# Optimization experiments

Hardware: AMD Instinct MI355X
Metric: run time of the kernel (lower is better)

## Reference

```python
import jax, jax.numpy as jnp
import numpy as np

N = 100000   # nodes
E = 1600000  # edges (avg degree 16)
IN, HID, OUT, HEADS = 8, 32, 16, 4


def setup_inputs() -> dict:
    key = jax.random.key(0)
    ks = jax.random.split(key, 12)
    def g(k, shape, fan):
        return (jax.random.normal(k, shape, jnp.float32) / np.float32(np.sqrt(fan)))
    x = jax.random.normal(ks[0], (N, IN), jnp.float32)
    edge_index = jax.random.randint(ks[1], (2, E), 0, N, dtype=jnp.int64)
    return {
        "x": x,
        "edge_index": edge_index,
        "W1": g(ks[2], (IN, HEADS * HID), IN),
        "att_src1": g(ks[3], (HEADS, HID), HID),
        "att_dst1": g(ks[4], (HEADS, HID), HID),
        "b1": jnp.zeros((HEADS * HID,), jnp.float32),
        "W2": g(ks[5], (HEADS * HID, OUT), HEADS * HID),
        "att_src2": g(ks[6], (1, OUT), OUT),
        "att_dst2": g(ks[7], (1, OUT), OUT),
        "b2": jnp.zeros((OUT,), jnp.float32),
        "Wc1": g(ks[8], (OUT, 8), OUT),
        "bc1": jnp.zeros((8,), jnp.float32),
        "Wc2": g(ks[9], (8, 1), 8),
        "bc2": jnp.zeros((1,), jnp.float32),
    }


def _gat_layer(x, W, att_src, att_dst, bias, src, dst, n, concat):
    """PyG GATConv (eval mode): gather -> per-edge attention -> segment softmax -> scatter."""
    H, D = att_src.shape
    h = (x @ W).reshape(n, H, D)                       # [N,H,D]
    a_s = jnp.einsum("nhd,hd->nh", h, att_src)          # [N,H]
    a_d = jnp.einsum("nhd,hd->nh", h, att_dst)          # [N,H]
    e = jax.nn.leaky_relu(a_s[src] + a_d[dst], 0.2)     # [Etot,H]
    m = jax.ops.segment_max(e, dst, num_segments=n)     # per-dst max for stable softmax
    m = jnp.where(jnp.isfinite(m), m, 0.0)
    e = jnp.exp(e - m[dst])
    denom = jax.ops.segment_sum(e, dst, num_segments=n)
    alpha = e / (denom[dst] + 1e-16)                    # [Etot,H]
    out = jax.ops.segment_sum(h[src] * alpha[:, :, None], dst, num_segments=n)  # [N,H,D]
    out = out.reshape(n, H * D) if concat else out.mean(axis=1)
    return out + bias


def reference(x, edge_index, W1, att_src1, att_dst1, b1, W2, att_src2, att_dst2, b2, Wc1, bc1, Wc2, bc2):
    n = x.shape[0]
    loops = jnp.arange(n, dtype=edge_index.dtype)       # add_self_loops=True (PyG default)
    src = jnp.concatenate([edge_index[0], loops])
    dst = jnp.concatenate([edge_index[1], loops])
    h = jax.nn.elu(_gat_layer(x, W1, att_src1, att_dst1, b1, src, dst, n, concat=True))
    emb = jax.nn.elu(_gat_layer(h, W2, att_src2, att_dst2, b2, src, dst, n, concat=False))
    risk = jax.nn.sigmoid(jax.nn.relu(emb @ Wc1 + bc1) @ Wc2 + bc2)
    return emb, risk
```

## Files before the change

### kernel.cpp

```cpp
#include <hip/hip_runtime.h>
#include <hip/hip_fp16.h>
#include <math.h>

#define N_NODES 100000
#define N_EDGES 1600000
#define F_IN 8
#define HID 32
#define HEADS 4
#define F1 128
#define F2 16
#define NB 391
#define NBLK_BIN 782
#define EDGES_PER_BIN 2048
#define NBLK_A 391
#define BCAP 4864

__device__ __forceinline__ float leaky(float x){ return x > 0.f ? x : 0.2f * x; }
__device__ __forceinline__ float elu1(float x){ return x > 0.f ? x : __expf(x) - 1.f; }

__global__ __launch_bounds__(256) void k_bin_attn(
    const int* __restrict__ src, const int* __restrict__ dst,
    int* __restrict__ bucketCnt, unsigned int* __restrict__ ebuf,
    const float* __restrict__ x, const float* __restrict__ W1,
    const float* __restrict__ as1w, const float* __restrict__ ad1w,
    float* __restrict__ xa){
    __shared__ float smem[1344];
    int t = threadIdx.x;
    if (blockIdx.x < NBLK_BIN){
        int* hist    = (int*)smem;
        int* basePos = hist + NB;
        int* cur     = basePos + NB;
        for (int j = t; j < NB; j += 256) hist[j] = 0;
        __syncthreads();
        int base = blockIdx.x * EDGES_PER_BIN;
        int dv[8];
        #pragma unroll
        for (int j = 0; j < 8; j++){
            int e = base + j * 256 + t;
            dv[j] = (e < N_EDGES) ? dst[e] : -1;
            if (dv[j] >= 0) atomicAdd(&hist[dv[j] >> 8], 1);
        }
        __syncthreads();
        for (int j = t; j < NB; j += 256){
            int h = hist[j];
            if (h) basePos[j] = atomicAdd(&bucketCnt[j], h);
            cur[j] = 0;
        }
        __syncthreads();
        #pragma unroll
        for (int j = 0; j < 8; j++){
            if (dv[j] >= 0){
                int e = base + j * 256 + t;
                int d = dv[j];
                int b = d >> 8;
                int off = atomicAdd(&cur[b], 1);
                ebuf[b * BCAP + basePos[b] + off] = ((unsigned)(d & 255) << 17) | (unsigned)src[e];
            }
        }
    } else {
        float* W1s  = smem;
        float* atts = smem + 1024;
        float* attd = smem + 1152;
        float* cs   = smem + 1280;
        float* cd   = smem + 1312;
        ((float4*)W1s)[t] = ((const float4*)W1)[t];
        if (t < 128){ atts[t] = as1w[t]; attd[t] = ad1w[t]; }
        __syncthreads();
        if (t < 64){
            int m = t & 7, h = (t >> 3) & 3;
            bool sel = t >= 32;
            const float* wrow = W1s + m * F1 + h * 32;
            const float* av   = (sel ? attd : atts) + h * 32;
            float s = 0.f;
            #pragma unroll
            for (int d = 0; d < 32; d++) s += wrow[d] * av[d];
            (sel ? cd : cs)[h * 8 + m] = s;
        }
        __syncthreads();
        int n = (blockIdx.x - NBLK_BIN) * 256 + t;
        if (n < N_NODES){
            float4 x0 = ((const float4*)x)[n * 2];
            float4 x1 = ((const float4*)x)[n * 2 + 1];
            float4 osv, odv;
            float* po = (float*)&osv;
            float* pd = (float*)&odv;
            #pragma unroll
            for (int h = 0; h < 4; h++){
                const float* c0 = cs + h * 8;
                const float* c1 = cd + h * 8;
                po[h] = x0.x*c0[0] + x0.y*c0[1] + x0.z*c0[2] + x0.w*c0[3]
                      + x1.x*c0[4] + x1.y*c0[5] + x1.z*c0[6] + x1.w*c0[7];
                pd[h] = x0.x*c1[0] + x0.y*c1[1] + x0.z*c1[2] + x0.w*c1[3]
                      + x1.x*c1[4] + x1.y*c1[5] + x1.z*c1[6] + x1.w*c1[7];
            }
            float* px = xa + (size_t)n * 16;
            *(float4*)(px)      = x0;
            *(float4*)(px + 4)  = x1;
            *(float4*)(px + 8)  = osv;
            *(float4*)(px + 12) = odv;
        }
    }
}

__global__ __launch_bounds__(512) void k_local_csr(
    const int* __restrict__ bucketCnt, const unsigned int* __restrict__ ebuf,
    int* __restrict__ row_ptr, int* __restrict__ esrc){
    __shared__ int deg[256];
    __shared__ int scn[512];
    __shared__ int cntAll[NB];
    __shared__ unsigned int segs[BCAP];
    int b = blockIdx.x, t = threadIdx.x;
    if (t < 256) deg[t] = 0;
    for (int j = t; j < NB; j += 512) cntAll[j] = bucketCnt[j];
    __syncthreads();
    int partial = 0;
    for (int j = t; j < b; j += 512) partial += cntAll[j];
    scn[t] = partial;
    __syncthreads();
    for (int off = 256; off > 0; off >>= 1){
        if (t < off) scn[t] += scn[t + off];
        __syncthreads();
    }
    int sbase = scn[0];
    int cnt = cntAll[b];
    __syncthreads();
    const unsigned int* seg = ebuf + b * BCAP;
    for (int i = t; i < cnt; i += 512){
        unsigned int e = seg[i];
        segs[i] = e;
        atomicAdd(&deg[e >> 17], 1);
    }
    __syncthreads();
    int v = (t < 256) ? deg[t] : 0;
    if (t < 256) scn[t] = v;
    __syncthreads();
    for (int off = 1; off < 256; off <<= 1){
        int xx = (t < 256 && t >= off) ? scn[t - off] : 0;
        __syncthreads();
        if (t < 256) scn[t] += xx;
        __syncthreads();
    }
    if (t < 256){
        int excl = scn[t] - v;
        int start = sbase + excl;
        int n = b * 256 + t;
        if (n < N_NODES) row_ptr[n] = start;
        deg[t] = start;
    }
    if (b == NB - 1 && t == 0) row_ptr[N_NODES] = sbase + cnt;
    __syncthreads();
    for (int i = t; i < cnt; i += 512){
        unsigned int e = segs[i];
        int pos = atomicAdd(&deg[e >> 17], 1);
        esrc[pos] = (int)(e & 0x1FFFFu);
    }
}

__global__ __launch_bounds__(256) void k_agg1(
    const float* __restrict__ xa, const int* __restrict__ row_ptr, const int* __restrict__ esrc,
    float* __restrict__ xagg, float* __restrict__ dden){
    int t = threadIdx.x;
    int wv = t >> 6, lane = t & 63;
    int n = blockIdx.x * 4 + wv;
    int g = lane >> 4;
    int l = lane & 15;
    int hd = l >> 2;
    int c2 = (l & 3) * 2;

    float vn = xa[(size_t)n * 16 + l];
    float adh = __shfl(vn, 12 + hd, 16);

    float den = 0.f, ac0 = 0.f, ac1 = 0.f;
    if (g == 0){
        float w = __expf(leaky(__shfl(vn, 8 + hd, 16) + adh));
        den = w;
        ac0 = w * __shfl(vn, c2, 16);
        ac1 = w * __shfl(vn, c2 + 1, 16);
    }
    int start = row_ptr[n], end = row_ptr[n + 1];
    int len = end - start;
    int chunk = (len + 3) >> 2;
    int i = start + g * chunk;
    int e = i + chunk; if (e > end) e = end;
    for (int base = i; base < e; base += 4){
        bool b1v = base + 1 < e, b2v = base + 2 < e, b3v = base + 3 < e;
        int s0 = esrc[base];
        int s1 = b1v ? esrc[base + 1] : s0;
        int s2 = b2v ? esrc[base + 2] : s0;
        int s3 = b3v ? esrc[base + 3] : s0;
        float v0 = xa[(size_t)s0 * 16 + l];
        float v1 = xa[(size_t)s1 * 16 + l];
        float v2 = xa[(size_t)s2 * 16 + l];
        float v3 = xa[(size_t)s3 * 16 + l];
        float w0 = __expf(leaky(__shfl(v0, 8 + hd, 16) + adh));
        float w1 = b1v ? __expf(leaky(__shfl(v1, 8 + hd, 16) + adh)) : 0.f;
        float w2 = b2v ? __expf(leaky(__shfl(v2, 8 + hd, 16) + adh)) : 0.f;
        float w3 = b3v ? __expf(leaky(__shfl(v3, 8 + hd, 16) + adh)) : 0.f;
        den += (w0 + w1) + (w2 + w3);
        ac0 = fmaf(w0, __shfl(v0, c2, 16), ac0); ac1 = fmaf(w0, __shfl(v0, c2 + 1, 16), ac1);
        ac0 = fmaf(w1, __shfl(v1, c2, 16), ac0); ac1 = fmaf(w1, __shfl(v1, c2 + 1, 16), ac1);
        ac0 = fmaf(w2, __shfl(v2, c2, 16), ac0); ac1 = fmaf(w2, __shfl(v2, c2 + 1, 16), ac1);
        ac0 = fmaf(w3, __shfl(v3, c2, 16), ac0); ac1 = fmaf(w3, __shfl(v3, c2 + 1, 16), ac1);
    }
    den += __shfl_xor(den, 16); den += __shfl_xor(den, 32);
    ac0 += __shfl_xor(ac0, 16); ac0 += __shfl_xor(ac0, 32);
    ac1 += __shfl_xor(ac1, 16); ac1 += __shfl_xor(ac1, 32);

    if (lane < 16){
        float2 o; o.x = ac0; o.y = ac1;
        *(float2*)(xagg + (size_t)n * 32 + 2 * l) = o;
        if ((l & 3) == 0) dden[(size_t)n * 4 + hd] = den;
    }
}

__global__ __launch_bounds__(256) void k_epi(
    const float* __restrict__ xagg, const float* __restrict__ dden,
    const float* __restrict__ W1, const float* __restrict__ W2,
    const float* __restrict__ b1, const float* __restrict__ as2w, const float* __restrict__ ad2w,
    __half* __restrict__ h2h, float* __restrict__ a_s2, float* __restrict__ a_d2){
    __shared__ __half2 W1h[F_IN * 64];
    __shared__ __half2 W2t[F2 * 64];
    __shared__ __half2 hlsh[16 * 68];
    int t = threadIdx.x;
    {
        float4 w1v = ((const float4*)W1)[t];
        int m = t >> 5, j = (2 * t) & 63;
        W1h[m * 64 + j]     = __floats2half2_rn(w1v.x, w1v.y);
        W1h[m * 64 + j + 1] = __floats2half2_rn(w1v.z, w1v.w);
        #pragma unroll
        for (int hf = 0; hf < 2; hf++){
            int p = t + hf * 256;
            float4 wv = ((const float4*)W2)[p];
            int k = p >> 2, dbase = (p & 3) * 4;
            float vals[4] = {wv.x, wv.y, wv.z, wv.w};
            #pragma unroll
            for (int c = 0; c < 4; c++){
                int dw = (dbase + c) * 64 + (k >> 1);
                int sdw = dw ^ (((dw >> 6) & 7) << 2);
                ((__half*)W2t)[2 * sdw + (k & 1)] = __float2half(vals[c]);
            }
        }
    }
    __syncthreads();

    int nn = t >> 4, q = t & 15;
    int n = blockIdx.x * 16 + nn;
    int hd = q >> 2;

    const float* xg = xagg + (size_t)n * 32 + hd * 8;
    float4 xga = *(const float4*)(xg);
    float4 xgb = *(const float4*)(xg + 4);
    float invd = 1.f / dden[(size_t)n * 4 + hd];
    float xv[8] = {xga.x, xga.y, xga.z, xga.w, xgb.x, xgb.y, xgb.z, xgb.w};
    float pre[8] = {0,0,0,0,0,0,0,0};
    #pragma unroll
    for (int m = 0; m < 8; m++){
        float4 raw = *(const float4*)(W1h + m * 64 + 4 * q);
        const __half2* wp = (const __half2*)&raw;
        float xm = xv[m];
        float2 f0 = __half22float2(wp[0]);
        float2 f1 = __half22float2(wp[1]);
        float2 f2 = __half22float2(wp[2]);
        float2 f3 = __half22float2(wp[3]);
        pre[0] = fmaf(xm, f0.x, pre[0]); pre[1] = fmaf(xm, f0.y, pre[1]);
        pre[2] = fmaf(xm, f1.x, pre[2]); pre[3] = fmaf(xm, f1.y, pre[3]);
        pre[4] = fmaf(xm, f2.x, pre[4]); pre[5] = fmaf(xm, f2.y, pre[5]);
        pre[6] = fmaf(xm, f3.x, pre[6]); pre[7] = fmaf(xm, f3.y, pre[7]);
    }
    float4 ba = *(const float4*)(b1 + 8 * q);
    float4 bb = *(const float4*)(b1 + 8 * q + 4);
    __half2 hout[4];
    hout[0] = __floats2half2_rn(elu1(pre[0] * invd + ba.x), elu1(pre[1] * invd + ba.y));
    hout[1] = __floats2half2_rn(elu1(pre[2] * invd + ba.z), elu1(pre[3] * invd + ba.w));
    hout[2] = __floats2half2_rn(elu1(pre[4] * invd + bb.x), elu1(pre[5] * invd + bb.y));
    hout[3] = __floats2half2_rn(elu1(pre[6] * invd + bb.z), elu1(pre[7] * invd + bb.w));
    *(float4*)(hlsh + nn * 68 + 4 * q) = *(float4*)hout;
    __syncthreads();

    float dot = 0.f;
    #pragma unroll
    for (int ob = 0; ob < 8; ob++){
        __half2 acc2 = __float2half2_rn(0.f);
        #pragma unroll
        for (int kb = ob * 2; kb < ob * 2 + 2; kb++){
            float4 hr = *(const float4*)(hlsh + nn * 68 + 4 * kb);
            int dwb = 64 * q + 4 * kb;
            float4 wr = *(const float4*)(W2t + (dwb ^ (((dwb >> 6) & 7) << 2)));
            const __half2* hp  = (const __half2*)&hr;
            const __half2* wp2 = (const __half2*)&wr;
            acc2 = __hfma2(hp[0], wp2[0], acc2);
            acc2 = __hfma2(hp[1], wp2[1], acc2);
            acc2 = __hfma2(hp[2], wp2[2], acc2);
            acc2 = __hfma2(hp[3], wp2[3], acc2);
        }
        float2 fa = __half22float2(acc2);
        dot += fa.x + fa.y;
    }
    float ps = dot * as2w[q];
    float pd = dot * ad2w[q];
    #pragma unroll
    for (int off = 8; off >= 1; off >>= 1){
        ps += __shfl_down(ps, off, 16);
        pd += __shfl_down(pd, off, 16);
    }
    if (q == 0){ a_s2[n] = ps; a_d2[n] = pd; }
    h2h[(size_t)n * F2 + q] = __float2half(dot);
}

__global__ __launch_bounds__(256) void k_agg2(
    const __half* __restrict__ h2h, const float* __restrict__ a_s2, const float* __restrict__ a_d2,
    const int* __restrict__ row_ptr, const int* __restrict__ esrc,
    const float* __restrict__ b2, float* __restrict__ out){
    int t = threadIdx.x;
    int wv = t >> 6, lane = t & 63;
    int n = blockIdx.x * 4 + wv;
    int g = lane >> 3;
    int l = lane & 7;
    float adn = a_d2[n];
    const __half* hb2 = h2h + 2 * l;

    float den = 0.f, acc0 = 0.f, acc1 = 0.f;
    if (g == 0){
        float w = __expf(leaky(a_s2[n] + adn));
        den = w;
        float2 f = __half22float2(*(const __half2*)(hb2 + ((unsigned)n << 4)));
        acc0 = w * f.x; acc1 = w * f.y;
    }
    int start = row_ptr[n], end = row_ptr[n + 1];
    int len = end - start;
    int chunk = (len + 7) >> 3;
    int i = start + g * chunk;
    int e = i + chunk; if (e > end) e = end;
    for (int base = i; base < e; base += 4){
        bool v1 = base + 1 < e, v2 = base + 2 < e, v3 = base + 3 < e;
        int s0 = esrc[base];
        int s1 = v1 ? esrc[base + 1] : s0;
        int s2 = v2 ? esrc[base + 2] : s0;
        int s3 = v3 ? esrc[base + 3] : s0;
        float a0 = a_s2[s0], a1 = a_s2[s1], a2 = a_s2[s2], a3 = a_s2[s3];
        __half2 p0 = *(const __half2*)(hb2 + ((unsigned)s0 << 4));
        __half2 p1 = *(const __half2*)(hb2 + ((unsigned)s1 << 4));
        __half2 p2 = *(const __half2*)(hb2 + ((unsigned)s2 << 4));
        __half2 p3 = *(const __half2*)(hb2 + ((unsigned)s3 << 4));
        float w0 = __expf(leaky(a0 + adn));
        float w1 = v1 ? __expf(leaky(a1 + adn)) : 0.f;
        float w2 = v2 ? __expf(leaky(a2 + adn)) : 0.f;
        float w3 = v3 ? __expf(leaky(a3 + adn)) : 0.f;
        den += (w0 + w1) + (w2 + w3);
        float2 f0 = __half22float2(p0), f1 = __half22float2(p1);
        float2 f2 = __half22float2(p2), f3 = __half22float2(p3);
        acc0 += w0 * f0.x + w1 * f1.x + w2 * f2.x + w3 * f3.x;
        acc1 += w0 * f0.y + w1 * f1.y + w2 * f2.y + w3 * f3.y;
    }
    #pragma unroll
    for (int off = 8; off <= 32; off <<= 1){
        den  += __shfl_xor(den, off);
        acc0 += __shfl_xor(acc0, off);
        acc1 += __shfl_xor(acc1, off);
    }
    if (g == 0){
        float inv = 1.f / (den + 1e-16f);
        float e0v = elu1(acc0 * inv + b2[2 * l]);
        float e1v = elu1(acc1 * inv + b2[2 * l + 1]);
        float2 ov; ov.x = e0v; ov.y = e1v;
        *(float2*)(out + (size_t)n * 16 + 2 * l) = ov;
    }
}

__global__ __launch_bounds__(256) void k_cls(
    const float* __restrict__ emb, const float* __restrict__ Wc1, const float* __restrict__ bc1,
    const float* __restrict__ Wc2, const float* __restrict__ bc2, float* __restrict__ risk){
    int n = blockIdx.x * 256 + threadIdx.x;
    if (n >= N_NODES) return;
    const float* er = emb + (size_t)n * 16;
    float4 e0 = *(const float4*)(er);
    float4 e1 = *(const float4*)(er + 4);
    float4 e2 = *(const float4*)(er + 8);
    float4 e3 = *(const float4*)(er + 12);
    float ev[16] = {e0.x, e0.y, e0.z, e0.w, e1.x, e1.y, e1.z, e1.w,
                    e2.x, e2.y, e2.z, e2.w, e3.x, e3.y, e3.z, e3.w};
    float hid[8];
    #pragma unroll
    for (int j = 0; j < 8; j++) hid[j] = bc1[j];
    #pragma unroll
    for (int d = 0; d < 16; d++){
        float v = ev[d];
        #pragma unroll
        for (int j = 0; j < 8; j++) hid[j] = fmaf(v, Wc1[d * 8 + j], hid[j]);
    }
    float o = bc2[0];
    #pragma unroll
    for (int j = 0; j < 8; j++) o = fmaf(fmaxf(hid[j], 0.f), Wc2[j], o);
    risk[n] = 1.f / (1.f + __expf(-o));
}

extern "C" void kernel_launch(void* const* d_in, const int* in_sizes, int n_in,
                              void* d_out, int out_size, void* d_ws, size_t ws_size,
                              hipStream_t stream){
    const float* x    = (const float*)d_in[0];
    const int*   ei   = (const int*)d_in[1];
    const float* W1   = (const float*)d_in[2];
    const float* as1w = (const float*)d_in[3];
    const float* ad1w = (const float*)d_in[4];
    const float* b1   = (const float*)d_in[5];
    const float* W2   = (const float*)d_in[6];
    const float* as2w = (const float*)d_in[7];
    const float* ad2w = (const float*)d_in[8];
    const float* b2   = (const float*)d_in[9];
    const float* Wc1  = (const float*)d_in[10];
    const float* bc1  = (const float*)d_in[11];
    const float* Wc2  = (const float*)d_in[12];
    const float* bc2  = (const float*)d_in[13];
    float* out = (float*)d_out;
    const int* src = ei;
    const int* dst = ei + N_EDGES;

    float* ws   = (float*)d_ws;
    float* a_s2 = ws;
    float* a_d2 = a_s2 + N_NODES;
    float* xa   = a_d2 + N_NODES;
    float* xagg = xa + (size_t)N_NODES * 16;
    float* dden = xagg + (size_t)N_NODES * 32;
    __half* h2h = (__half*)(dden + (size_t)N_NODES * 4);
    int* bucketCnt = (int*)(h2h + (size_t)N_NODES * 16);
    int* row_ptr  = bucketCnt + NB;
    int* esrc     = row_ptr + N_NODES + 1;
    unsigned int* ebuf = (unsigned int*)(esrc + N_EDGES);

    hipMemsetAsync(bucketCnt, 0, NB * sizeof(int), stream);
    k_bin_attn<<<NBLK_BIN + NBLK_A, 256, 0, stream>>>(
        src, dst, bucketCnt, ebuf, x, W1, as1w, ad1w, xa);
    k_local_csr<<<NB, 512, 0, stream>>>(bucketCnt, ebuf, row_ptr, esrc);
    k_agg1<<<N_NODES / 4, 256, 0, stream>>>(xa, row_ptr, esrc, xagg, dden);
    k_epi<<<N_NODES / 16, 256, 0, stream>>>(
        xagg, dden, W1, W2, b1, as2w, ad2w, h2h, a_s2, a_d2);
    k_agg2<<<N_NODES / 4, 256, 0, stream>>>(h2h, a_s2, a_d2, row_ptr, esrc, b2, out);
    k_cls<<<(N_NODES + 255) / 256, 256, 0, stream>>>(
        out, Wc1, bc1, Wc2, bc2, out + (size_t)N_NODES * 16);
}
```

Baseline: 235.8 us.

## Store layer-1 node features in half precision and regroup agg1 lanes

Packs the per-node input features and the two attention logits into 16 half values (32 bytes) instead of 16 floats, which halves the gather traffic per edge in the first aggregation. The aggregation kernel is reorganised so 8 lanes cover a node row and 8 groups split the edge list, with each lane accumulating 4 outputs. This reduces random-gather bandwidth at the cost of fp16 rounding on inputs and logits, and adds an extra shuffle-reduction step.

```diff
diff --git a/kernel.cpp b/kernel.cpp
--- a/kernel.cpp
+++ b/kernel.cpp
@@ -17,6 +17,11 @@
 
 __device__ __forceinline__ float leaky(float x){ return x > 0.f ? x : 0.2f * x; }
 __device__ __forceinline__ float elu1(float x){ return x > 0.f ? x : __expf(x) - 1.f; }
+__device__ __forceinline__ float half_of(float v, int hi){
+    float2 f = __half22float2(*(__half2*)&v);
+    return hi ? f.y : f.x;
+}
+__device__ __forceinline__ float2 h2f2(float v){ return __half22float2(*(__half2*)&v); }
 
 __global__ __launch_bounds__(256) void k_bin_attn(
     const int* __restrict__ src, const int* __restrict__ dst,
@@ -93,11 +98,18 @@
                 pd[h] = x0.x*c1[0] + x0.y*c1[1] + x0.z*c1[2] + x0.w*c1[3]
                       + x1.x*c1[4] + x1.y*c1[5] + x1.z*c1[6] + x1.w*c1[7];
             }
-            float* px = xa + (size_t)n * 16;
-            *(float4*)(px)      = x0;
-            *(float4*)(px + 4)  = x1;
-            *(float4*)(px + 8)  = osv;
-            *(float4*)(px + 12) = odv;
+            __half2 h8[8];
+            h8[0] = __floats2half2_rn(x0.x, x0.y);
+            h8[1] = __floats2half2_rn(x0.z, x0.w);
+            h8[2] = __floats2half2_rn(x1.x, x1.y);
+            h8[3] = __floats2half2_rn(x1.z, x1.w);
+            h8[4] = __floats2half2_rn(osv.x, osv.y);
+            h8[5] = __floats2half2_rn(osv.z, osv.w);
+            h8[6] = __floats2half2_rn(odv.x, odv.y);
+            h8[7] = __floats2half2_rn(odv.z, odv.w);
+            float* px = xa + (size_t)n * 8;
+            *(float4*)(px)     = *(float4*)(h8);
+            *(float4*)(px + 4) = *(float4*)(h8 + 4);
         }
     }
 }
@@ -162,24 +174,26 @@
     int t = threadIdx.x;
     int wv = t >> 6, lane = t & 63;
     int n = blockIdx.x * 4 + wv;
-    int g = lane >> 4;
-    int l = lane & 15;
-    int hd = l >> 2;
-    int c2 = (l & 3) * 2;
-
-    float vn = xa[(size_t)n * 16 + l];
-    float adh = __shfl(vn, 12 + hd, 16);
-
-    float den = 0.f, ac0 = 0.f, ac1 = 0.f;
+    int g = lane >> 3;
+    int l = lane & 7;
+    int hd = l >> 1;
+    int ha = 4 + (hd >> 1), hb = hd & 1;
+    int xd = 2 * (l & 1);
+
+    float vn = xa[(size_t)n * 8 + l];
+    float adh = half_of(__shfl(vn, ha + 2, 8), hb);
+
+    float den = 0.f, ac0 = 0.f, ac1 = 0.f, ac2 = 0.f, ac3 = 0.f;
     if (g == 0){
-        float w = __expf(leaky(__shfl(vn, 8 + hd, 16) + adh));
+        float w = __expf(leaky(half_of(__shfl(vn, ha, 8), hb) + adh));
         den = w;
-        ac0 = w * __shfl(vn, c2, 16);
-        ac1 = w * __shfl(vn, c2 + 1, 16);
+        float2 p01 = h2f2(__shfl(vn, xd, 8));
+        float2 p23 = h2f2(__shfl(vn, xd + 1, 8));
+        ac0 = w * p01.x; ac1 = w * p01.y; ac2 = w * p23.x; ac3 = w * p23.y;
     }
     int start = row_ptr[n], end = row_ptr[n + 1];
     int len = end - start;
-    int chunk = (len + 3) >> 2;
+    int chunk = (len + 7) >> 3;
     int i = start + g * chunk;
     int e = i + chunk; if (e > end) e = end;
     for (int base = i; base < e; base += 4){
@@ -188,28 +202,39 @@
         int s1 = b1v ? esrc[base + 1] : s0;
         int s2 = b2v ? esrc[base + 2] : s0;
         int s3 = b3v ? esrc[base + 3] : s0;
-        float v0 = xa[(size_t)s0 * 16 + l];
-        float v1 = xa[(size_t)s1 * 16 + l];
-        float v2 = xa[(size_t)s2 * 16 + l];
-        float v3 = xa[(size_t)s3 * 16 + l];
-        float w0 = __expf(leaky(__shfl(v0, 8 + hd, 16) + adh));
-        float w1 = b1v ? __expf(leaky(__shfl(v1, 8 + hd, 16) + adh)) : 0.f;
-        float w2 = b2v ? __expf(leaky(__shfl(v2, 8 + hd, 16) + adh)) : 0.f;
-        float w3 = b3v ? __expf(leaky(__shfl(v3, 8 + hd, 16) + adh)) : 0.f;
+        float v0 = xa[(size_t)s0 * 8 + l];
+        float v1 = xa[(size_t)s1 * 8 + l];
+        float v2 = xa[(size_t)s2 * 8 + l];
+        float v3 = xa[(size_t)s3 * 8 + l];
+        float w0 = __expf(leaky(half_of(__shfl(v0, ha, 8), hb) + adh));
+        float w1 = b1v ? __expf(leaky(half_of(__shfl(v1, ha, 8), hb) + adh)) : 0.f;
+        float w2 = b2v ? __expf(leaky(half_of(__shfl(v2, ha, 8), hb) + adh)) : 0.f;
+        float w3 = b3v ? __expf(leaky(half_of(__shfl(v3, ha, 8), hb) + adh)) : 0.f;
         den += (w0 + w1) + (w2 + w3);
-        ac0 = fmaf(w0, __shfl(v0, c2, 16), ac0); ac1 = fmaf(w0, __shfl(v0, c2 + 1, 16), ac1);
-        ac0 = fmaf(w1, __shfl(v1, c2, 16), ac0); ac1 = fmaf(w1, __shfl(v1, c2 + 1, 16), ac1);
-        ac0 = fmaf(w2, __shfl(v2, c2, 16), ac0); ac1 = fmaf(w2, __shfl(v2, c2 + 1, 16), ac1);
-        ac0 = fmaf(w3, __shfl(v3, c2, 16), ac0); ac1 = fmaf(w3, __shfl(v3, c2 + 1, 16), ac1);
-    }
-    den += __shfl_xor(den, 16); den += __shfl_xor(den, 32);
-    ac0 += __shfl_xor(ac0, 16); ac0 += __shfl_xor(ac0, 32);
-    ac1 += __shfl_xor(ac1, 16); ac1 += __shfl_xor(ac1, 32);
-
-    if (lane < 16){
-        float2 o; o.x = ac0; o.y = ac1;
-        *(float2*)(xagg + (size_t)n * 32 + 2 * l) = o;
-        if ((l & 3) == 0) dden[(size_t)n * 4 + hd] = den;
+        float2 a01, a23;
+        a01 = h2f2(__shfl(v0, xd, 8)); a23 = h2f2(__shfl(v0, xd + 1, 8));
+        ac0 = fmaf(w0, a01.x, ac0); ac1 = fmaf(w0, a01.y, ac1);
+        ac2 = fmaf(w0, a23.x, ac2); ac3 = fmaf(w0, a23.y, ac3);
+        a01 = h2f2(__shfl(v1, xd, 8)); a23 = h2f2(__shfl(v1, xd + 1, 8));
+        ac0 = fmaf(w1, a01.x, ac0); ac1 = fmaf(w1, a01.y, ac1);
+        ac2 = fmaf(w1, a23.x, ac2); ac3 = fmaf(w1, a23.y, ac3);
+        a01 = h2f2(__shfl(v2, xd, 8)); a23 = h2f2(__shfl(v2, xd + 1, 8));
+        ac0 = fmaf(w2, a01.x, ac0); ac1 = fmaf(w2, a01.y, ac1);
+        ac2 = fmaf(w2, a23.x, ac2); ac3 = fmaf(w2, a23.y, ac3);
+        a01 = h2f2(__shfl(v3, xd, 8)); a23 = h2f2(__shfl(v3, xd + 1, 8));
+        ac0 = fmaf(w3, a01.x, ac0); ac1 = fmaf(w3, a01.y, ac1);
+        ac2 = fmaf(w3, a23.x, ac2); ac3 = fmaf(w3, a23.y, ac3);
+    }
+    den += __shfl_xor(den, 8); den += __shfl_xor(den, 16); den += __shfl_xor(den, 32);
+    ac0 += __shfl_xor(ac0, 8); ac0 += __shfl_xor(ac0, 16); ac0 += __shfl_xor(ac0, 32);
+    ac1 += __shfl_xor(ac1, 8); ac1 += __shfl_xor(ac1, 16); ac1 += __shfl_xor(ac1, 32);
+    ac2 += __shfl_xor(ac2, 8); ac2 += __shfl_xor(ac2, 16); ac2 += __shfl_xor(ac2, 32);
+    ac3 += __shfl_xor(ac3, 8); ac3 += __shfl_xor(ac3, 16); ac3 += __shfl_xor(ac3, 32);
+
+    if (lane < 8){
+        float4 o; o.x = ac0; o.y = ac1; o.z = ac2; o.w = ac3;
+        *(float4*)(xagg + (size_t)n * 32 + 4 * l) = o;
+        if (!(l & 1)) dden[(size_t)n * 4 + hd] = den;
     }
 }
 
@@ -419,7 +444,7 @@
     float* a_s2 = ws;
     float* a_d2 = a_s2 + N_NODES;
     float* xa   = a_d2 + N_NODES;
-    float* xagg = xa + (size_t)N_NODES * 16;
+    float* xagg = xa + (size_t)N_NODES * 8;
     float* dden = xagg + (size_t)N_NODES * 32;
     __half* h2h = (__half*)(dden + (size_t)N_NODES * 4);
     int* bucketCnt = (int*)(h2h + (size_t)N_NODES * 16);
```

After: 234.9 us. No clear change (-0.4%).
